# Kernel optimization log

Measured on AMD Instinct MI355X. Metric: run time of the kernel, lower is better.

Reference implementation:

```python
import jax, jax.numpy as jnp
import numpy as np

B, T, C = 4, 2048, 1024
N_HEAD = 16
HEAD_DIM = C // N_HEAD


def setup_inputs() -> dict:
    key = jax.random.key(0)
    k1, k2, k3 = jax.random.split(key, 3)
    scale = 1.0 / np.sqrt(C)
    return {
        "x": jax.random.normal(k1, (B, T, C), dtype=jnp.float32),
        "W_attn": jax.random.normal(k2, (C, 3 * C), dtype=jnp.float32) * scale,
        "b_attn": jnp.zeros((3 * C,), dtype=jnp.float32),
        "W_proj": jax.random.normal(k3, (C, C), dtype=jnp.float32) * scale,
        "b_proj": jnp.zeros((C,), dtype=jnp.float32),
    }


def reference(x, W_attn, b_attn, W_proj, b_proj):
    Bt, Tt, Ct = x.shape
    qkv = x @ W_attn + b_attn                      # [B,T,3C]
    q, k, v = jnp.split(qkv, 3, axis=-1)
    # [B,T,C] -> [B,H,T,D]
    def heads(t):
        return t.reshape(Bt, Tt, N_HEAD, HEAD_DIM).transpose(0, 2, 1, 3)
    q, k, v = heads(q), heads(k), heads(v)
    att = jnp.einsum("bhqd,bhkd->bhqk", q, k) * (1.0 / np.sqrt(HEAD_DIM))
    causal = jnp.tril(jnp.ones((Tt, Tt), dtype=bool))
    att = jnp.where(causal, att, jnp.finfo(att.dtype).min)
    att = jax.nn.softmax(att, axis=-1)
    # dropout = 0.0 (eval mode): identity
    y = jnp.einsum("bhqk,bhkd->bhqd", att, v)      # [B,H,T,D]
    y = y.transpose(0, 2, 1, 3).reshape(Bt, Tt, Ct)
    return y @ W_proj + b_proj
```

## Files before the change

kernel.cpp:

```cpp
#include <hip/hip_runtime.h>
#include <hip/hip_bf16.h>
#include <cstdint>

#define B_SZ 4
#define T_SZ 2048
#define C_SZ 1024
#define H_SZ 16
#define D_SZ 64
#define BT_SZ (B_SZ * T_SZ)
#define C3_SZ (3 * C_SZ)
#define NKC (C_SZ / 32)

typedef __attribute__((ext_vector_type(8))) short bf16x8;
typedef __attribute__((ext_vector_type(4))) float f32x4;
typedef __attribute__((ext_vector_type(4))) unsigned short ushort4v;
typedef __attribute__((ext_vector_type(4))) unsigned int uint4v;

__device__ __forceinline__ unsigned short f2bf(float f) {
  unsigned u = __builtin_bit_cast(unsigned, f);
  u += 0x7fffu + ((u >> 16) & 1u);
  return (unsigned short)(u >> 16);
}

__device__ __forceinline__ unsigned packbf2(float lo, float hi) {
  return __builtin_amdgcn_perm(__builtin_bit_cast(unsigned, hi),
                               __builtin_bit_cast(unsigned, lo), 0x07060302u);
}


__global__ __launch_bounds__(256) void pack_x(const float* __restrict__ x,
                                              unsigned short* __restrict__ Af) {
  const int task = blockIdx.x * 4 + (threadIdx.x >> 6);
  const int lane = threadIdx.x & 63;
  const int quad = lane >> 4, n = lane & 15;
  const int tb = task >> 5, kc = task & 31;
  const float* src = x + (size_t)(tb * 16 + n) * C_SZ + kc * 32 + quad * 8;
  float4 a = *(const float4*)src;
  float4 b = *(const float4*)(src + 4);
  ushort4v o0, o1;
  o0[0] = f2bf(a.x); o0[1] = f2bf(a.y); o0[2] = f2bf(a.z); o0[3] = f2bf(a.w);
  o1[0] = f2bf(b.x); o1[1] = f2bf(b.y); o1[2] = f2bf(b.z); o1[3] = f2bf(b.w);
  unsigned short* dst = Af + ((size_t)((tb * NKC + kc) * 4 + quad) * 16 + n) * 8;
  *(ushort4v*)dst = o0;
  *(ushort4v*)(dst + 4) = o1;
}

__global__ __launch_bounds__(256) void pack_w(const float* __restrict__ W,
                                              unsigned short* __restrict__ Wb,
                                              int N) {
  const int task = blockIdx.x * 4 + (threadIdx.x >> 6);
  const int lane = threadIdx.x & 63;
  const int quad = lane >> 4, n = lane & 15;
  const int nt = task >> 5, kc = task & 31;
  const int col = nt * 16 + n;
  const int k0 = kc * 32 + quad * 8;
  ushort4v o0, o1;
#pragma unroll
  for (int i = 0; i < 4; ++i) o0[i] = f2bf(W[(size_t)(k0 + i) * N + col]);
#pragma unroll
  for (int i = 0; i < 4; ++i) o1[i] = f2bf(W[(size_t)(k0 + 4 + i) * N + col]);
  unsigned short* dst = Wb + ((size_t)((nt * NKC + kc) * 4 + quad) * 16 + n) * 8;
  *(ushort4v*)dst = o0;
  *(ushort4v*)(dst + 4) = o1;
}

#define GEMM_MAINLOOP(Ap, Bp, tb0, nt0, quad, n, acc)                         \
  _Pragma("unroll 2") for (int kc = 0; kc < NKC; ++kc) {                      \
    bf16x8 af[4], bfr[4];                                                     \
    _Pragma("unroll") for (int m = 0; m < 4; ++m)                             \
        af[m] = Ap[((size_t)((tb0 + m) * NKC + kc) * 4 + quad) * 16 + n];     \
    _Pragma("unroll") for (int nn = 0; nn < 4; ++nn)                          \
        bfr[nn] = Bp[((size_t)((nt0 + nn) * NKC + kc) * 4 + quad) * 16 + n];  \
    _Pragma("unroll") for (int m = 0; m < 4; ++m)                             \
        _Pragma("unroll") for (int nn = 0; nn < 4; ++nn)                      \
            acc[m][nn] = __builtin_amdgcn_mfma_f32_16x16x32_bf16(             \
                af[m], bfr[nn], acc[m][nn], 0, 0, 0);                         \
  }

__global__ __launch_bounds__(256) void qkv_mfma(
    const unsigned short* __restrict__ Af, const unsigned short* __restrict__ Wab,
    const float* __restrict__ bias, unsigned short* __restrict__ Qf,
    unsigned short* __restrict__ Kf, unsigned short* __restrict__ Vf) {
  const int tid = threadIdx.x;
  const int w = tid >> 6, lane = tid & 63;
  const int quad = lane >> 4, n = lane & 15;
  const int wr = w >> 1, wc = w & 1;
  const int bx = blockIdx.x, by = blockIdx.y;
  const int tb0 = by * 8 + wr * 4;
  const int nt0 = bx * 8 + wc * 4;
  const bf16x8* Ap = (const bf16x8*)Af;
  const bf16x8* Bp = (const bf16x8*)Wab;
  f32x4 acc[4][4];
#pragma unroll
  for (int m = 0; m < 4; ++m)
#pragma unroll
    for (int nn = 0; nn < 4; ++nn) acc[m][nn] = (f32x4){0.f, 0.f, 0.f, 0.f};

  GEMM_MAINLOOP(Ap, Bp, tb0, nt0, quad, n, acc)

  const int cb = bx * 128 + wc * 64;
  const int which = cb >> 10;
  const int h = (cb & 1023) >> 6;
  const int gr0 = by * 128 + wr * 64;
  const int b = gr0 >> 11;
  const int t0 = gr0 & 2047;
  const size_t bhoff = (size_t)(b * H_SZ + h) * (T_SZ * D_SZ);
  float bfl[4];
#pragma unroll
  for (int nn = 0; nn < 4; ++nn) bfl[nn] = bias[cb + nn * 16 + n];

  if (which < 2) {
    unsigned short* dst = ((which == 0) ? Qf : Kf) + bhoff;
    const float scl = (which == 0) ? 0.18033688f : 1.0f;
#pragma unroll
    for (int m = 0; m < 4; ++m) {
      const int tb = (t0 + m * 16) >> 4;
#pragma unroll
      for (int nn = 0; nn < 4; ++nn) {
        const int dc = nn >> 1;
        const int qd = (nn & 1) * 2 + (n >> 3);
        const int jq = n & 7;
#pragma unroll
        for (int r = 0; r < 4; ++r) {
          const int nq = quad * 4 + r;
          dst[((size_t)((tb * 2 + dc) * 4 + qd)) * 128 + nq * 8 + jq] =
              f2bf((acc[m][nn][r] + bfl[nn]) * scl);
        }
      }
    }
  } else {
    unsigned short* dst = Vf + bhoff;
    const int gb0 = t0 >> 5;
#pragma unroll
    for (int m = 0; m < 4; ++m) {
      const int gb = gb0 + (m >> 1);
#pragma unroll
      for (int nn = 0; nn < 4; ++nn) {
#pragma unroll
        for (int r = 0; r < 4; ++r) {
          dst[((size_t)((gb * 4 + nn) * 4 + quad)) * 128 + n * 8 + (m & 1) * 4 + r] =
              f2bf(acc[m][nn][r] + bfl[nn]);
        }
      }
    }
  }
}

__global__ __launch_bounds__(256) void proj_mfma(
    const unsigned short* __restrict__ Yf, const unsigned short* __restrict__ Wpb,
    const float* __restrict__ bias, float* __restrict__ out) {
  const int tid = threadIdx.x;
  const int w = tid >> 6, lane = tid & 63;
  const int quad = lane >> 4, n = lane & 15;
  const int wr = w >> 1, wc = w & 1;
  const int bx = blockIdx.x, by = blockIdx.y;
  const int tb0 = by * 8 + wr * 4;
  const int nt0 = bx * 8 + wc * 4;
  const bf16x8* Ap = (const bf16x8*)Yf;
  const bf16x8* Bp = (const bf16x8*)Wpb;
  f32x4 acc[4][4];
#pragma unroll
  for (int m = 0; m < 4; ++m)
#pragma unroll
    for (int nn = 0; nn < 4; ++nn) acc[m][nn] = (f32x4){0.f, 0.f, 0.f, 0.f};

  GEMM_MAINLOOP(Ap, Bp, tb0, nt0, quad, n, acc)

  const int cb = bx * 128 + wc * 64;
  const int gr0 = by * 128 + wr * 64;
  float bfl[4];
#pragma unroll
  for (int nn = 0; nn < 4; ++nn) bfl[nn] = bias[cb + nn * 16 + n];
#pragma unroll
  for (int m = 0; m < 4; ++m)
#pragma unroll
    for (int nn = 0; nn < 4; ++nn)
#pragma unroll
      for (int r = 0; r < 4; ++r)
        out[(size_t)(gr0 + m * 16 + quad * 4 + r) * C_SZ + cb + nn * 16 + n] =
            acc[m][nn][r] + bfl[nn];
}

__global__ __launch_bounds__(64) void attn_mfma(
    const unsigned short* __restrict__ Qf,
    const unsigned short* __restrict__ Kf,
    const unsigned short* __restrict__ Vf, unsigned short* __restrict__ Yf) {
  const int lane = threadIdx.x;
  const int quad = lane >> 4;
  const int n = lane & 15;
  const int bx = blockIdx.x;
  const int qt = 31 - (bx >> 6);
  const int bh = bx & 63;
  const int b = bh >> 4, h = bh & 15;
  const int wq0 = qt * 64;
  const size_t bhoff = (size_t)bh * (T_SZ * D_SZ);
  const bf16x8* Qp = (const bf16x8*)(Qf + bhoff);
  const bf16x8* Kp = (const bf16x8*)(Kf + bhoff);
  const bf16x8* Vp = (const bf16x8*)(Vf + bhoff);

  bf16x8 qfr[4][2];
#pragma unroll
  for (int m = 0; m < 4; ++m) {
    const int tb = (wq0 >> 4) + m;
#pragma unroll
    for (int dc = 0; dc < 2; ++dc)
      qfr[m][dc] = Qp[((tb * 2 + dc) * 4 + quad) * 16 + n];
  }

  f32x4 O[4][4];
  f32x4 ls[4];
#pragma unroll
  for (int m = 0; m < 4; ++m) {
    ls[m] = (f32x4){0.f, 0.f, 0.f, 0.f};
#pragma unroll
    for (int dv = 0; dv < 4; ++dv) O[m][dv] = (f32x4){0.f, 0.f, 0.f, 0.f};
  }

  for (int kt = 0; kt < qt; ++kt) {
    const int k0 = kt * 64;
    bf16x8 kfr[4][2], vfr[2][4];
#pragma unroll
    for (int s = 0; s < 4; ++s) {
      const int tb = (k0 >> 4) + s;
      kfr[s][0] = Kp[((tb * 2 + 0) * 4 + quad) * 16 + n];
      kfr[s][1] = Kp[((tb * 2 + 1) * 4 + quad) * 16 + n];
    }
#pragma unroll
    for (int g = 0; g < 2; ++g) {
      const int gb = (k0 >> 5) + g;
#pragma unroll
      for (int dv = 0; dv < 4; ++dv)
        vfr[g][dv] = Vp[((gb * 4 + dv) * 4 + quad) * 16 + n];
    }
#pragma unroll
    for (int m = 0; m < 4; ++m) {
      f32x4 st[4];
#pragma unroll
      for (int s = 0; s < 4; ++s) {
        f32x4 z = {0.f, 0.f, 0.f, 0.f};
        z = __builtin_amdgcn_mfma_f32_16x16x32_bf16(kfr[s][0], qfr[m][0], z, 0, 0, 0);
        z = __builtin_amdgcn_mfma_f32_16x16x32_bf16(kfr[s][1], qfr[m][1], z, 0, 0, 0);
        st[s] = z;
      }
      uint4v pw[2];
#pragma unroll
      for (int s = 0; s < 4; ++s) {
        float pr[4];
#pragma unroll
        for (int r = 0; r < 4; ++r) {
          pr[r] = __builtin_amdgcn_exp2f(st[s][r]);
          ls[m][r] += pr[r];
        }
        pw[s >> 1][(s & 1) * 2 + 0] = packbf2(pr[0], pr[1]);
        pw[s >> 1][(s & 1) * 2 + 1] = packbf2(pr[2], pr[3]);
      }
#pragma unroll
      for (int g = 0; g < 2; ++g) {
        const bf16x8 pg = __builtin_bit_cast(bf16x8, pw[g]);
#pragma unroll
        for (int dv = 0; dv < 4; ++dv)
          O[m][dv] = __builtin_amdgcn_mfma_f32_16x16x32_bf16(
              pg, vfr[g][dv], O[m][dv], 0, 0, 0);
      }
    }
  }

  {
    const int k0 = wq0;
    bf16x8 kfr[4][2], vfr[2][4];
#pragma unroll
    for (int s = 0; s < 4; ++s) {
      const int tb = (k0 >> 4) + s;
      kfr[s][0] = Kp[((tb * 2 + 0) * 4 + quad) * 16 + n];
      kfr[s][1] = Kp[((tb * 2 + 1) * 4 + quad) * 16 + n];
    }
#pragma unroll
    for (int g = 0; g < 2; ++g) {
      const int gb = (k0 >> 5) + g;
#pragma unroll
      for (int dv = 0; dv < 4; ++dv)
        vfr[g][dv] = Vp[((gb * 4 + dv) * 4 + quad) * 16 + n];
    }
#pragma unroll
    for (int m = 0; m < 4; ++m) {
      f32x4 st[4];
#pragma unroll
      for (int s = 0; s < 4; ++s) {
        f32x4 z = {0.f, 0.f, 0.f, 0.f};
        if (s <= m) {
          z = __builtin_amdgcn_mfma_f32_16x16x32_bf16(kfr[s][0], qfr[m][0], z, 0, 0, 0);
          z = __builtin_amdgcn_mfma_f32_16x16x32_bf16(kfr[s][1], qfr[m][1], z, 0, 0, 0);
        }
        st[s] = z;
      }
      uint4v pw[2] = {(uint4v){0, 0, 0, 0}, (uint4v){0, 0, 0, 0}};
#pragma unroll
      for (int s = 0; s < 4; ++s) {
        if (s <= m) {
          float pr[4];
#pragma unroll
          for (int r = 0; r < 4; ++r) {
            float v = st[s][r];
            if (s == m && quad * 4 + r > n) v = -1e30f;
            pr[r] = __builtin_amdgcn_exp2f(v);
            ls[m][r] += pr[r];
          }
          pw[s >> 1][(s & 1) * 2 + 0] = packbf2(pr[0], pr[1]);
          pw[s >> 1][(s & 1) * 2 + 1] = packbf2(pr[2], pr[3]);
        }
      }
#pragma unroll
      for (int g = 0; g < 2; ++g) {
        if (g * 2 <= m) {
          const bf16x8 pg = __builtin_bit_cast(bf16x8, pw[g]);
#pragma unroll
          for (int dv = 0; dv < 4; ++dv)
            O[m][dv] = __builtin_amdgcn_mfma_f32_16x16x32_bf16(
                pg, vfr[g][dv], O[m][dv], 0, 0, 0);
        }
      }
    }
  }

#pragma unroll
  for (int m = 0; m < 4; ++m) {
    float lt = ls[m][0] + ls[m][1] + ls[m][2] + ls[m][3];
    lt += __shfl_xor(lt, 16);
    lt += __shfl_xor(lt, 32);
    const float inv = 1.0f / lt;
    float iv[4];
#pragma unroll
    for (int r = 0; r < 4; ++r) iv[r] = __shfl(inv, quad * 4 + r);
    const int tb = (b * T_SZ + wq0 + m * 16) >> 4;
#pragma unroll
    for (int dv = 0; dv < 4; ++dv) {
      const int kc = h * 2 + (dv >> 1);
      const int qa = (dv & 1) * 2 + (n >> 3);
      const int ja = n & 7;
#pragma unroll
      for (int r = 0; r < 4; ++r) {
        const int na = quad * 4 + r;
        Yf[((size_t)((tb * NKC + kc) * 4 + qa)) * 128 + na * 8 + ja] =
            f2bf(O[m][dv][r] * iv[r]);
      }
    }
  }
}

extern "C" void kernel_launch(void* const* d_in, const int* in_sizes, int n_in,
                              void* d_out, int out_size, void* d_ws,
                              size_t ws_size, hipStream_t stream) {
  const float* x = (const float*)d_in[0];
  const float* W_attn = (const float*)d_in[1];
  const float* b_attn = (const float*)d_in[2];
  const float* W_proj = (const float*)d_in[3];
  const float* b_proj = (const float*)d_in[4];
  float* out = (float*)d_out;

  const size_t perbf = (size_t)B_SZ * H_SZ * T_SZ * D_SZ;
  unsigned short* Af = (unsigned short*)d_ws;
  unsigned short* Wab = Af + (size_t)BT_SZ * C_SZ;
  unsigned short* Wpb = Wab + (size_t)C_SZ * C3_SZ;
  unsigned short* Qf = Wpb + (size_t)C_SZ * C_SZ;
  unsigned short* Kf = Qf + perbf;
  unsigned short* Vf = Kf + perbf;
  unsigned short* Yf = Vf + perbf;

  pack_x<<<(BT_SZ / 16) * NKC / 4, 256, 0, stream>>>(x, Af);
  pack_w<<<(C3_SZ / 16) * NKC / 4, 256, 0, stream>>>(W_attn, Wab, C3_SZ);
  pack_w<<<(C_SZ / 16) * NKC / 4, 256, 0, stream>>>(W_proj, Wpb, C_SZ);
  qkv_mfma<<<dim3(C3_SZ / 128, BT_SZ / 128), 256, 0, stream>>>(
      Af, Wab, b_attn, Qf, Kf, Vf);
  attn_mfma<<<dim3(32 * B_SZ * H_SZ), 64, 0, stream>>>(Qf, Kf, Vf, Yf);
  proj_mfma<<<dim3(C_SZ / 128, BT_SZ / 128), 256, 0, stream>>>(Yf, Wpb, b_proj,
                                                               out);
}
```

Measured before the change: 257.8 us.

## Stage GEMM tiles in LDS via direct global-to-LDS loads

```diff
diff --git a/kernel.cpp b/kernel.cpp
--- a/kernel.cpp
+++ b/kernel.cpp
@@ -16,6 +16,9 @@
 typedef __attribute__((ext_vector_type(4))) unsigned short ushort4v;
 typedef __attribute__((ext_vector_type(4))) unsigned int uint4v;
 
+typedef __attribute__((address_space(3))) unsigned int lds_u32;
+typedef __attribute__((address_space(1))) const unsigned int glb_u32;
+
 __device__ __forceinline__ unsigned short f2bf(float f) {
   unsigned u = __builtin_bit_cast(unsigned, f);
   u += 0x7fffu + ((u >> 16) & 1u);
@@ -25,6 +28,11 @@
 __device__ __forceinline__ unsigned packbf2(float lo, float hi) {
   return __builtin_amdgcn_perm(__builtin_bit_cast(unsigned, hi),
                                __builtin_bit_cast(unsigned, lo), 0x07060302u);
+}
+
+__device__ __forceinline__ void gll16(const unsigned short* g,
+                                      unsigned short* l) {
+  __builtin_amdgcn_global_load_lds((glb_u32*)g, (lds_u32*)l, 16, 0, 0);
 }
 
 
@@ -64,39 +72,69 @@
   *(ushort4v*)(dst + 4) = o1;
 }
 
-#define GEMM_MAINLOOP(Ap, Bp, tb0, nt0, quad, n, acc)                         \
-  _Pragma("unroll 2") for (int kc = 0; kc < NKC; ++kc) {                      \
-    bf16x8 af[4], bfr[4];                                                     \
-    _Pragma("unroll") for (int m = 0; m < 4; ++m)                             \
-        af[m] = Ap[((size_t)((tb0 + m) * NKC + kc) * 4 + quad) * 16 + n];     \
-    _Pragma("unroll") for (int nn = 0; nn < 4; ++nn)                          \
-        bfr[nn] = Bp[((size_t)((nt0 + nn) * NKC + kc) * 4 + quad) * 16 + n];  \
-    _Pragma("unroll") for (int m = 0; m < 4; ++m)                             \
-        _Pragma("unroll") for (int nn = 0; nn < 4; ++nn)                      \
-            acc[m][nn] = __builtin_amdgcn_mfma_f32_16x16x32_bf16(             \
-                af[m], bfr[nn], acc[m][nn], 0, 0, 0);                         \
-  }
+__device__ __forceinline__ void gemm128_mainloop(
+    const unsigned short* __restrict__ A, const unsigned short* __restrict__ B,
+    int tbB, int ntB, unsigned short* smem, f32x4 acc[4][4]) {
+  const int tid = threadIdx.x;
+  const int w = tid >> 6, lane = tid & 63;
+  const int quad = lane >> 4, n = lane & 15;
+  const int wr = w >> 1, wc = w & 1;
+  unsigned short* smemA = smem;
+  unsigned short* smemB = smem + 8192;
+
+  for (int kc0 = 0; kc0 < NKC; kc0 += 2) {
+#pragma unroll
+    for (int i2 = 0; i2 < 2; ++i2) {
+      const int i = 2 * w + i2;
+      const unsigned short* gA =
+          A + ((size_t)(tbB + i) * NKC + kc0) * 512 + lane * 8;
+      const unsigned short* gB =
+          B + ((size_t)(ntB + i) * NKC + kc0) * 512 + lane * 8;
+      gll16(gA, smemA + i * 1024);
+      gll16(gA + 512, smemA + i * 1024 + 512);
+      gll16(gB, smemB + i * 1024);
+      gll16(gB + 512, smemB + i * 1024 + 512);
+    }
+    __syncthreads();
+#pragma unroll
+    for (int kcl = 0; kcl < 2; ++kcl) {
+      bf16x8 af[4], bfr[4];
+#pragma unroll
+      for (int m = 0; m < 4; ++m)
+        af[m] = *(const bf16x8*)(smemA + (wr * 4 + m) * 1024 +
+                                 (kcl * 4 + quad) * 128 + n * 8);
+#pragma unroll
+      for (int nn = 0; nn < 4; ++nn)
+        bfr[nn] = *(const bf16x8*)(smemB + (wc * 4 + nn) * 1024 +
+                                   (kcl * 4 + quad) * 128 + n * 8);
+#pragma unroll
+      for (int m = 0; m < 4; ++m)
+#pragma unroll
+        for (int nn = 0; nn < 4; ++nn)
+          acc[m][nn] = __builtin_amdgcn_mfma_f32_16x16x32_bf16(
+              af[m], bfr[nn], acc[m][nn], 0, 0, 0);
+    }
+    __syncthreads();
+  }
+}
 
 __global__ __launch_bounds__(256) void qkv_mfma(
     const unsigned short* __restrict__ Af, const unsigned short* __restrict__ Wab,
     const float* __restrict__ bias, unsigned short* __restrict__ Qf,
     unsigned short* __restrict__ Kf, unsigned short* __restrict__ Vf) {
+  __shared__ unsigned short smem[16384];
   const int tid = threadIdx.x;
   const int w = tid >> 6, lane = tid & 63;
   const int quad = lane >> 4, n = lane & 15;
   const int wr = w >> 1, wc = w & 1;
   const int bx = blockIdx.x, by = blockIdx.y;
-  const int tb0 = by * 8 + wr * 4;
-  const int nt0 = bx * 8 + wc * 4;
-  const bf16x8* Ap = (const bf16x8*)Af;
-  const bf16x8* Bp = (const bf16x8*)Wab;
   f32x4 acc[4][4];
 #pragma unroll
   for (int m = 0; m < 4; ++m)
 #pragma unroll
     for (int nn = 0; nn < 4; ++nn) acc[m][nn] = (f32x4){0.f, 0.f, 0.f, 0.f};
 
-  GEMM_MAINLOOP(Ap, Bp, tb0, nt0, quad, n, acc)
+  gemm128_mainloop(Af, Wab, by * 8, bx * 8, smem, acc);
 
   const int cb = bx * 128 + wc * 64;
   const int which = cb >> 10;
@@ -149,22 +187,19 @@
 __global__ __launch_bounds__(256) void proj_mfma(
     const unsigned short* __restrict__ Yf, const unsigned short* __restrict__ Wpb,
     const float* __restrict__ bias, float* __restrict__ out) {
+  __shared__ unsigned short smem[16384];
   const int tid = threadIdx.x;
   const int w = tid >> 6, lane = tid & 63;
   const int quad = lane >> 4, n = lane & 15;
   const int wr = w >> 1, wc = w & 1;
   const int bx = blockIdx.x, by = blockIdx.y;
-  const int tb0 = by * 8 + wr * 4;
-  const int nt0 = bx * 8 + wc * 4;
-  const bf16x8* Ap = (const bf16x8*)Yf;
-  const bf16x8* Bp = (const bf16x8*)Wpb;
   f32x4 acc[4][4];
 #pragma unroll
   for (int m = 0; m < 4; ++m)
 #pragma unroll
     for (int nn = 0; nn < 4; ++nn) acc[m][nn] = (f32x4){0.f, 0.f, 0.f, 0.f};
 
-  GEMM_MAINLOOP(Ap, Bp, tb0, nt0, quad, n, acc)
+  gemm128_mainloop(Yf, Wpb, by * 8, bx * 8, smem, acc);
 
   const int cb = bx * 128 + wc * 64;
   const int gr0 = by * 128 + wr * 64;
```

Result: faster. 237.6 us (-7.8%).
